# Kernel tuning notes

Hardware: AMD Instinct MI355X
Metric: run time of the kernel (lower is better)

Reference implementation:

```python
import jax, jax.numpy as jnp
import numpy as np

N, IN_DIM, HEADS, C = 100000, 128, 4, 32  # out_dim = HEADS*C = 128
E = 1600000


def setup_inputs() -> dict:
    key = jax.random.key(0)
    ks = jax.random.split(key, 9)
    x = jax.random.normal(ks[0], (N, IN_DIM), dtype=jnp.float32)
    edge_index = jax.random.randint(ks[1], (2, E), 0, N, dtype=jnp.int64)
    # GATConv params
    W = jax.random.normal(ks[2], (HEADS * C, IN_DIM), dtype=jnp.float32) * (1.0 / np.sqrt(IN_DIM))
    att_src = jax.random.normal(ks[3], (HEADS, C), dtype=jnp.float32) * 0.1
    att_dst = jax.random.normal(ks[4], (HEADS, C), dtype=jnp.float32) * 0.1
    bias = jax.random.normal(ks[5], (HEADS * C,), dtype=jnp.float32) * 0.01
    # complex phase + LayerNorm params
    phase = jax.random.normal(ks[6], (HEADS * C,), dtype=jnp.float32) * 0.02
    gamma = 1.0 + jax.random.normal(ks[7], (HEADS * C,), dtype=jnp.float32) * 0.01
    beta = jax.random.normal(ks[8], (HEADS * C,), dtype=jnp.float32) * 0.01
    return {"x": x, "edge_index": edge_index, "W": W, "att_src": att_src,
            "att_dst": att_dst, "bias": bias, "phase": phase, "gamma": gamma, "beta": beta}


def reference(x, edge_index, W, att_src, att_dst, bias, phase, gamma, beta):
    src, dst = edge_index[0], edge_index[1]
    h = (x @ W.T).reshape(N, HEADS, C)                      # [N,H,C]
    a_src = jnp.einsum('nhc,hc->nh', h, att_src)            # [N,H]
    a_dst = jnp.einsum('nhc,hc->nh', h, att_dst)
    e = jax.nn.leaky_relu(a_src[src] + a_dst[dst], 0.2)     # [E,H]
    # segment softmax over destination nodes (numerically stable)
    m = jax.ops.segment_max(e, dst, num_segments=N)         # [N,H]
    ex = jnp.exp(e - m[dst])
    s = jax.ops.segment_sum(ex, dst, num_segments=N)        # [N,H]
    alpha = ex / (s[dst] + 1e-16)                           # [E,H]
    msg = h[src] * alpha[:, :, None]                        # [E,H,C]
    out = jax.ops.segment_sum(msg, dst, num_segments=N).reshape(N, HEADS * C) + bias
    # complex phase magnitude: sqrt((h cos p)^2 + (h sin p)^2 + eps)
    mag = jnp.sqrt((out * jnp.cos(phase)) ** 2 + (out * jnp.sin(phase)) ** 2 + 1e-12)
    # LayerNorm
    mu = mag.mean(-1, keepdims=True)
    var = ((mag - mu) ** 2).mean(-1, keepdims=True)
    hn = (mag - mu) / jnp.sqrt(var + 1e-5) * gamma + beta
    return jax.nn.gelu(hn, approximate=False)
```

## Files before the change

### kernel.cpp

```cpp
#include <hip/hip_runtime.h>
#include <hip/hip_bf16.h>

#define N_ 100000
#define E_ 1600000
#define D_ 128
#define H_ 4
#define C_ 32

using bf16 = __hip_bfloat16;
typedef __attribute__((ext_vector_type(8))) short short8;
typedef __attribute__((ext_vector_type(4))) float f32x4;

__device__ __forceinline__ float u2f(unsigned u) { return __uint_as_float(u); }
__device__ __forceinline__ unsigned short f2bu(float v) {
  bf16 t = __float2bfloat16(v);
  return *(unsigned short*)&t;
}

__global__ __launch_bounds__(256) void k_linear_mfma(
    const float* __restrict__ x, const float* __restrict__ W,
    const float* __restrict__ att_src, const float* __restrict__ att_dst,
    bf16* __restrict__ h, float* __restrict__ a_src, float* __restrict__ a_dst) {
  __shared__ unsigned short WB[16384];
  __shared__ unsigned short XS[64 * 128];
  __shared__ float ats[128], atd[128];
  const int tid = threadIdx.x;
  const int lane = tid & 63, w = tid >> 6;
  const int n15 = lane & 15, quad = lane >> 4;

  for (int i = tid; i < 16384; i += 256) {
    const int n = i >> 7, k = i & 127;
    const int kk = k >> 5, q = (k >> 3) & 3, j = k & 7;
    const int frag = kk * 8 + (n >> 4);
    WB[frag * 512 + q * 128 + (n & 15) * 8 + j] = f2bu(W[n * 128 + k]);
  }
  if (tid < 128) { ats[tid] = att_src[tid]; atd[tid] = att_dst[tid]; }

  const int nrb = (N_ + 63) / 64;
  for (int rb = blockIdx.x; rb < nrb; rb += gridDim.x) {
    const int row0 = rb * 64;
    __syncthreads();
    for (int idx = tid; idx < 2048; idx += 256) {
      const int r = idx >> 5;
      const int c = (idx & 31) * 4;
      float4 xv = make_float4(0.f, 0.f, 0.f, 0.f);
      if (row0 + r < N_) xv = *(const float4*)&x[(size_t)(row0 + r) * 128 + c];
      ushort4 o;
      o.x = f2bu(xv.x); o.y = f2bu(xv.y); o.z = f2bu(xv.z); o.w = f2bu(xv.w);
      *(ushort4*)&XS[r * 128 + c] = o;
    }
    __syncthreads();

    f32x4 acc[8] = {};
    const int arow = w * 16 + n15;
#pragma unroll
    for (int kk = 0; kk < 4; kk++) {
      const short8 a = *(const short8*)&XS[arow * 128 + kk * 32 + quad * 8];
#pragma unroll
      for (int t = 0; t < 8; t++) {
        const short8 b = *(const short8*)&WB[(kk * 8 + t) * 512 + lane * 8];
        acc[t] = __builtin_amdgcn_mfma_f32_16x16x32_bf16(a, b, acc[t], 0, 0, 0);
      }
    }

    __syncthreads();
#pragma unroll
    for (int t = 0; t < 8; t++)
#pragma unroll
      for (int reg = 0; reg < 4; reg++)
        XS[(w * 16 + quad * 4 + reg) * 128 + t * 16 + n15] =
            f2bu(acc[t][reg]);
    __syncthreads();
    {
      const int row = tid >> 2;
      const int hd = tid & 3;
      const int cb = hd * 32;
      const int grow = row0 + row;
      float ps = 0.f, pd = 0.f;
      if (grow < N_) {
#pragma unroll
        for (int g = 0; g < 4; g++) {
          const uint4 v = *(const uint4*)&XS[row * 128 + cb + g * 8];
          *(uint4*)&h[(size_t)grow * 128 + cb + g * 8] = v;
          const unsigned uu[4] = {v.x, v.y, v.z, v.w};
#pragma unroll
          for (int p = 0; p < 4; p++) {
            const float f0 = u2f(uu[p] << 16);
            const float f1 = u2f(uu[p] & 0xffff0000u);
            const int cc = cb + g * 8 + p * 2;
            ps = fmaf(f0, ats[cc], ps);     ps = fmaf(f1, ats[cc + 1], ps);
            pd = fmaf(f0, atd[cc], pd);     pd = fmaf(f1, atd[cc + 1], pd);
          }
        }
        a_src[grow * 4 + hd] = ps;
        a_dst[grow * 4 + hd] = pd;
      }
    }
  }
}

__global__ __launch_bounds__(256) void k_link(const int* __restrict__ ei,
                                              int* __restrict__ head4,
                                              int* __restrict__ nxt) {
  const int e = blockIdx.x * 256 + threadIdx.x;
  if (e >= E_) return;
  const int d = ei[E_ + e];
  const int prev = atomicExch(&head4[d * 4 + (e & 3)], e);
  nxt[e] = prev;
}

__global__ __launch_bounds__(256) void k_gather_ll(
    const int* __restrict__ head4, const int* __restrict__ nxt,
    const int* __restrict__ ei, const float* __restrict__ a_src,
    const float* __restrict__ a_dst, const bf16* __restrict__ h,
    const float* __restrict__ bias, const float* __restrict__ phase,
    const float* __restrict__ gamma, const float* __restrict__ beta,
    float* __restrict__ out) {
  const int lane = threadIdx.x & 63;
  const int d = blockIdx.x * 4 + (threadIdx.x >> 6);
  if (d >= N_) return;
  const int head = lane >> 4;
  const float ad = a_dst[d * 4 + head];
  const int ch = lane * 2;

  int e0 = head4[d * 4 + 0], e1 = head4[d * 4 + 1];
  int e2 = head4[d * 4 + 2], e3 = head4[d * 4 + 3];

  float acc0 = 0.f, acc1 = 0.f, sumw = 0.f;
  while ((e0 & e1 & e2 & e3) != -1) {
    const int c0 = (e0 < 0) ? 0 : e0, c1 = (e1 < 0) ? 0 : e1;
    const int c2 = (e2 < 0) ? 0 : e2, c3 = (e3 < 0) ? 0 : e3;
    const int n0 = nxt[c0], n1 = nxt[c1], n2 = nxt[c2], n3 = nxt[c3];
    const int s0 = ei[c0], s1 = ei[c1], s2 = ei[c2], s3 = ei[c3];
    const __hip_bfloat162 h0 = *(const __hip_bfloat162*)&h[s0 * 128 + ch];
    const __hip_bfloat162 h1 = *(const __hip_bfloat162*)&h[s1 * 128 + ch];
    const __hip_bfloat162 h2 = *(const __hip_bfloat162*)&h[s2 * 128 + ch];
    const __hip_bfloat162 h3 = *(const __hip_bfloat162*)&h[s3 * 128 + ch];
    const float as0 = a_src[s0 * 4 + head], as1 = a_src[s1 * 4 + head];
    const float as2 = a_src[s2 * 4 + head], as3 = a_src[s3 * 4 + head];

    float v0 = as0 + ad; v0 = (v0 > 0.f) ? v0 : 0.2f * v0;
    float v1 = as1 + ad; v1 = (v1 > 0.f) ? v1 : 0.2f * v1;
    float v2 = as2 + ad; v2 = (v2 > 0.f) ? v2 : 0.2f * v2;
    float v3 = as3 + ad; v3 = (v3 > 0.f) ? v3 : 0.2f * v3;
    const float w0 = (e0 < 0) ? 0.f : __expf(v0);
    const float w1 = (e1 < 0) ? 0.f : __expf(v1);
    const float w2 = (e2 < 0) ? 0.f : __expf(v2);
    const float w3 = (e3 < 0) ? 0.f : __expf(v3);

    acc0 = fmaf(w0, __low2float(h0), acc0);
    acc1 = fmaf(w0, __high2float(h0), acc1);
    acc0 = fmaf(w1, __low2float(h1), acc0);
    acc1 = fmaf(w1, __high2float(h1), acc1);
    acc0 = fmaf(w2, __low2float(h2), acc0);
    acc1 = fmaf(w2, __high2float(h2), acc1);
    acc0 = fmaf(w3, __low2float(h3), acc0);
    acc1 = fmaf(w3, __high2float(h3), acc1);
    sumw += (w0 + w1) + (w2 + w3);

    e0 = (e0 < 0) ? -1 : n0;
    e1 = (e1 < 0) ? -1 : n1;
    e2 = (e2 < 0) ? -1 : n2;
    e3 = (e3 < 0) ? -1 : n3;
  }

  const float inv = 1.0f / (sumw + 1e-16f);
  const float2 bi = *(const float2*)&bias[ch];
  const float2 ph = *(const float2*)&phase[ch];
  const float v0 = acc0 * inv + bi.x;
  const float v1 = acc1 * inv + bi.y;
  float sp, cp;
  sincosf(ph.x, &sp, &cp);
  const float m0 = sqrtf(v0 * v0 * (cp * cp + sp * sp) + 1e-12f);
  sincosf(ph.y, &sp, &cp);
  const float m1 = sqrtf(v1 * v1 * (cp * cp + sp * sp) + 1e-12f);

  float s1 = m0 + m1;
#pragma unroll
  for (int off = 32; off > 0; off >>= 1) s1 += __shfl_xor(s1, off);
  const float mu = s1 * (1.0f / 128.0f);
  const float d0 = m0 - mu, d1 = m1 - mu;
  float q = d0 * d0 + d1 * d1;
#pragma unroll
  for (int off = 32; off > 0; off >>= 1) q += __shfl_xor(q, off);
  const float rstd = rsqrtf(q * (1.0f / 128.0f) + 1e-5f);
  const float2 ga = *(const float2*)&gamma[ch];
  const float2 be = *(const float2*)&beta[ch];
  const float hn0 = d0 * rstd * ga.x + be.x;
  const float hn1 = d1 * rstd * ga.y + be.y;
  const float g0 = 0.5f * hn0 * (1.0f + erff(hn0 * 0.70710678118654752f));
  const float g1 = 0.5f * hn1 * (1.0f + erff(hn1 * 0.70710678118654752f));
  *(float2*)&out[d * 128 + ch] = make_float2(g0, g1);
}

extern "C" void kernel_launch(void* const* d_in, const int* in_sizes, int n_in,
                              void* d_out, int out_size, void* d_ws, size_t ws_size,
                              hipStream_t stream) {
  const float* x       = (const float*)d_in[0];
  const int*   ei      = (const int*)d_in[1];
  const float* W       = (const float*)d_in[2];
  const float* att_src = (const float*)d_in[3];
  const float* att_dst = (const float*)d_in[4];
  const float* bias    = (const float*)d_in[5];
  const float* phase   = (const float*)d_in[6];
  const float* gamma   = (const float*)d_in[7];
  const float* beta    = (const float*)d_in[8];
  float* out = (float*)d_out;

  bf16*  h     = (bf16*)d_ws;
  float* a_src = (float*)(h + (size_t)N_ * D_);
  float* a_dst = a_src + (size_t)N_ * H_;
  int*   head4 = (int*)(a_dst + (size_t)N_ * H_);
  int*   nxt   = head4 + (size_t)N_ * 4;

  hipMemsetAsync(head4, 0xFF, (size_t)N_ * 4 * sizeof(int), stream);

  k_linear_mfma<<<768, 256, 0, stream>>>(x, W, att_src, att_dst, h, a_src,
                                         a_dst);
  k_link<<<(E_ + 255) / 256, 256, 0, stream>>>(ei, head4, nxt);
  k_gather_ll<<<(N_ + 3) / 4, 256, 0, stream>>>(head4, nxt, ei, a_src, a_dst,
                                                h, bias, phase, gamma, beta,
                                                out);
}
```

Measured before the change: 340.0 us.

## Use 8 linked-list chains per node with packed src/next and wide row loads

Edge linked lists are split into 8 chains per destination instead of 4. The source index and next pointer are packed into one int2 so each hop needs a single load. In the gather, each of 8 lane groups walks one chain and loads 32-byte chunks of the h row, then the groups are combined with shuffle reductions. The phase sin/cos term is dropped because cos²+sin²=1, which leaves more parallel pointer chasing per node but adds register pressure and cross-lane reduction cost.

Result: slower. 358.0 us (+5.3%).

```diff
diff --git a/kernel.cpp b/kernel.cpp
--- a/kernel.cpp
+++ b/kernel.cpp
@@ -100,97 +100,101 @@
 }
 
 __global__ __launch_bounds__(256) void k_link(const int* __restrict__ ei,
-                                              int* __restrict__ head4,
-                                              int* __restrict__ nxt) {
+                                              int* __restrict__ head8,
+                                              int2* __restrict__ nxt2) {
   const int e = blockIdx.x * 256 + threadIdx.x;
   if (e >= E_) return;
   const int d = ei[E_ + e];
-  const int prev = atomicExch(&head4[d * 4 + (e & 3)], e);
-  nxt[e] = prev;
-}
-
-__global__ __launch_bounds__(256) void k_gather_ll(
-    const int* __restrict__ head4, const int* __restrict__ nxt,
-    const int* __restrict__ ei, const float* __restrict__ a_src,
-    const float* __restrict__ a_dst, const bf16* __restrict__ h,
-    const float* __restrict__ bias, const float* __restrict__ phase,
+  const int prev = atomicExch(&head8[d * 8 + (e & 7)], e);
+  nxt2[e] = make_int2(ei[e], prev);
+}
+
+__global__ __launch_bounds__(256) void k_gather8(
+    const int* __restrict__ head8, const int2* __restrict__ nxt2,
+    const float* __restrict__ a_src, const float* __restrict__ a_dst,
+    const bf16* __restrict__ h, const float* __restrict__ bias,
     const float* __restrict__ gamma, const float* __restrict__ beta,
     float* __restrict__ out) {
   const int lane = threadIdx.x & 63;
   const int d = blockIdx.x * 4 + (threadIdx.x >> 6);
   if (d >= N_) return;
-  const int head = lane >> 4;
+  const int j = lane >> 3;
+  const int cg = lane & 7;
+  const int head = cg >> 1;
   const float ad = a_dst[d * 4 + head];
-  const int ch = lane * 2;
-
-  int e0 = head4[d * 4 + 0], e1 = head4[d * 4 + 1];
-  int e2 = head4[d * 4 + 2], e3 = head4[d * 4 + 3];
-
-  float acc0 = 0.f, acc1 = 0.f, sumw = 0.f;
-  while ((e0 & e1 & e2 & e3) != -1) {
-    const int c0 = (e0 < 0) ? 0 : e0, c1 = (e1 < 0) ? 0 : e1;
-    const int c2 = (e2 < 0) ? 0 : e2, c3 = (e3 < 0) ? 0 : e3;
-    const int n0 = nxt[c0], n1 = nxt[c1], n2 = nxt[c2], n3 = nxt[c3];
-    const int s0 = ei[c0], s1 = ei[c1], s2 = ei[c2], s3 = ei[c3];
-    const __hip_bfloat162 h0 = *(const __hip_bfloat162*)&h[s0 * 128 + ch];
-    const __hip_bfloat162 h1 = *(const __hip_bfloat162*)&h[s1 * 128 + ch];
-    const __hip_bfloat162 h2 = *(const __hip_bfloat162*)&h[s2 * 128 + ch];
-    const __hip_bfloat162 h3 = *(const __hip_bfloat162*)&h[s3 * 128 + ch];
-    const float as0 = a_src[s0 * 4 + head], as1 = a_src[s1 * 4 + head];
-    const float as2 = a_src[s2 * 4 + head], as3 = a_src[s3 * 4 + head];
-
-    float v0 = as0 + ad; v0 = (v0 > 0.f) ? v0 : 0.2f * v0;
-    float v1 = as1 + ad; v1 = (v1 > 0.f) ? v1 : 0.2f * v1;
-    float v2 = as2 + ad; v2 = (v2 > 0.f) ? v2 : 0.2f * v2;
-    float v3 = as3 + ad; v3 = (v3 > 0.f) ? v3 : 0.2f * v3;
-    const float w0 = (e0 < 0) ? 0.f : __expf(v0);
-    const float w1 = (e1 < 0) ? 0.f : __expf(v1);
-    const float w2 = (e2 < 0) ? 0.f : __expf(v2);
-    const float w3 = (e3 < 0) ? 0.f : __expf(v3);
-
-    acc0 = fmaf(w0, __low2float(h0), acc0);
-    acc1 = fmaf(w0, __high2float(h0), acc1);
-    acc0 = fmaf(w1, __low2float(h1), acc0);
-    acc1 = fmaf(w1, __high2float(h1), acc1);
-    acc0 = fmaf(w2, __low2float(h2), acc0);
-    acc1 = fmaf(w2, __high2float(h2), acc1);
-    acc0 = fmaf(w3, __low2float(h3), acc0);
-    acc1 = fmaf(w3, __high2float(h3), acc1);
-    sumw += (w0 + w1) + (w2 + w3);
-
-    e0 = (e0 < 0) ? -1 : n0;
-    e1 = (e1 < 0) ? -1 : n1;
-    e2 = (e2 < 0) ? -1 : n2;
-    e3 = (e3 < 0) ? -1 : n3;
+
+  int e = head8[d * 8 + j];
+  float acc[16];
+#pragma unroll
+  for (int k = 0; k < 16; k++) acc[k] = 0.f;
+  float sumw = 0.f;
+
+  while (__any(e != -1)) {
+    const int c = (e < 0) ? 0 : e;
+    const int2 sn = nxt2[c];
+    const int s = sn.x;
+    const uint4 u0 = *(const uint4*)&h[(size_t)s * 128 + cg * 16];
+    const uint4 u1 = *(const uint4*)&h[(size_t)s * 128 + cg * 16 + 8];
+    float ev = a_src[s * 4 + head] + ad;
+    ev = (ev > 0.f) ? ev : 0.2f * ev;
+    const float w = (e < 0) ? 0.f : __expf(ev);
+    const unsigned uu[8] = {u0.x, u0.y, u0.z, u0.w, u1.x, u1.y, u1.z, u1.w};
+#pragma unroll
+    for (int p = 0; p < 8; p++) {
+      acc[p * 2]     = fmaf(w, u2f(uu[p] << 16), acc[p * 2]);
+      acc[p * 2 + 1] = fmaf(w, u2f(uu[p] & 0xffff0000u), acc[p * 2 + 1]);
+    }
+    sumw += w;
+    e = (e < 0) ? -1 : sn.y;
+  }
+
+#pragma unroll
+  for (int off = 8; off <= 32; off <<= 1) {
+#pragma unroll
+    for (int k = 0; k < 16; k++) acc[k] += __shfl_xor(acc[k], off);
+    sumw += __shfl_xor(sumw, off);
   }
 
   const float inv = 1.0f / (sumw + 1e-16f);
-  const float2 bi = *(const float2*)&bias[ch];
-  const float2 ph = *(const float2*)&phase[ch];
-  const float v0 = acc0 * inv + bi.x;
-  const float v1 = acc1 * inv + bi.y;
-  float sp, cp;
-  sincosf(ph.x, &sp, &cp);
-  const float m0 = sqrtf(v0 * v0 * (cp * cp + sp * sp) + 1e-12f);
-  sincosf(ph.y, &sp, &cp);
-  const float m1 = sqrtf(v1 * v1 * (cp * cp + sp * sp) + 1e-12f);
-
-  float s1 = m0 + m1;
-#pragma unroll
-  for (int off = 32; off > 0; off >>= 1) s1 += __shfl_xor(s1, off);
-  const float mu = s1 * (1.0f / 128.0f);
-  const float d0 = m0 - mu, d1 = m1 - mu;
-  float q = d0 * d0 + d1 * d1;
-#pragma unroll
-  for (int off = 32; off > 0; off >>= 1) q += __shfl_xor(q, off);
+  float biv[16], gav[16], bev[16];
+#pragma unroll
+  for (int g = 0; g < 4; g++) {
+    *(float4*)&biv[g * 4] = *(const float4*)&bias[cg * 16 + g * 4];
+    *(float4*)&gav[g * 4] = *(const float4*)&gamma[cg * 16 + g * 4];
+    *(float4*)&bev[g * 4] = *(const float4*)&beta[cg * 16 + g * 4];
+  }
+
+  float m[16], part = 0.f;
+#pragma unroll
+  for (int k = 0; k < 16; k++) {
+    const float v = acc[k] * inv + biv[k];
+    m[k] = sqrtf(v * v + 1e-12f);
+    part += m[k];
+  }
+#pragma unroll
+  for (int off = 1; off <= 4; off <<= 1) part += __shfl_xor(part, off);
+  const float mu = part * (1.0f / 128.0f);
+  float q = 0.f;
+#pragma unroll
+  for (int k = 0; k < 16; k++) {
+    m[k] -= mu;
+    q += m[k] * m[k];
+  }
+#pragma unroll
+  for (int off = 1; off <= 4; off <<= 1) q += __shfl_xor(q, off);
   const float rstd = rsqrtf(q * (1.0f / 128.0f) + 1e-5f);
-  const float2 ga = *(const float2*)&gamma[ch];
-  const float2 be = *(const float2*)&beta[ch];
-  const float hn0 = d0 * rstd * ga.x + be.x;
-  const float hn1 = d1 * rstd * ga.y + be.y;
-  const float g0 = 0.5f * hn0 * (1.0f + erff(hn0 * 0.70710678118654752f));
-  const float g1 = 0.5f * hn1 * (1.0f + erff(hn1 * 0.70710678118654752f));
-  *(float2*)&out[d * 128 + ch] = make_float2(g0, g1);
+
+  float o[16];
+#pragma unroll
+  for (int k = 0; k < 16; k++) {
+    const float hn = m[k] * rstd * gav[k] + bev[k];
+    o[k] = 0.5f * hn * (1.0f + erff(hn * 0.70710678118654752f));
+  }
+  if (lane < 8) {
+#pragma unroll
+    for (int g = 0; g < 4; g++)
+      *(float4*)&out[(size_t)d * 128 + cg * 16 + g * 4] = *(float4*)&o[g * 4];
+  }
 }
 
 extern "C" void kernel_launch(void* const* d_in, const int* in_sizes, int n_in,
@@ -202,7 +206,6 @@
   const float* att_src = (const float*)d_in[3];
   const float* att_dst = (const float*)d_in[4];
   const float* bias    = (const float*)d_in[5];
-  const float* phase   = (const float*)d_in[6];
   const float* gamma   = (const float*)d_in[7];
   const float* beta    = (const float*)d_in[8];
   float* out = (float*)d_out;
@@ -210,15 +213,14 @@
   bf16*  h     = (bf16*)d_ws;
   float* a_src = (float*)(h + (size_t)N_ * D_);
   float* a_dst = a_src + (size_t)N_ * H_;
-  int*   head4 = (int*)(a_dst + (size_t)N_ * H_);
-  int*   nxt   = head4 + (size_t)N_ * 4;
-
-  hipMemsetAsync(head4, 0xFF, (size_t)N_ * 4 * sizeof(int), stream);
+  int*   head8 = (int*)(a_dst + (size_t)N_ * H_);
+  int2*  nxt2  = (int2*)(head8 + (size_t)N_ * 8);
+
+  hipMemsetAsync(head8, 0xFF, (size_t)N_ * 8 * sizeof(int), stream);
 
   k_linear_mfma<<<768, 256, 0, stream>>>(x, W, att_src, att_dst, h, a_src,
                                          a_dst);
-  k_link<<<(E_ + 255) / 256, 256, 0, stream>>>(ei, head4, nxt);
-  k_gather_ll<<<(N_ + 3) / 4, 256, 0, stream>>>(head4, nxt, ei, a_src, a_dst,
-                                                h, bias, phase, gamma, beta,
-                                                out);
-}
+  k_link<<<(E_ + 255) / 256, 256, 0, stream>>>(ei, head8, nxt2);
+  k_gather8<<<(N_ + 3) / 4, 256, 0, stream>>>(head8, nxt2, a_src, a_dst, h,
+                                              bias, gamma, beta, out);
+}
```

## Pack src index with next link and distribute list walks across lanes

Applied to the files above, without the earlier changes.

Stores the source index together with the next-edge link as one int2 per edge, so a single load per hop replaces two dependent loads. The gather kernel assigns lanes 0-3 to walk the four linked lists, computes each edge's weight once, and broadcasts the weights and source offsets with shuffles instead of having every lane reload the same list entries. It also drops the sin/cos phase computation, since cos^2+sin^2 = 1 algebraically. The trade-off is shuffle overhead per hop and divergence when the list lengths differ, and the cos^2+sin^2 rounding difference from the reference is ignored.

New measurement: 340.6 us. No clear change (+0.2%).

```diff
diff --git a/kernel.cpp b/kernel.cpp
--- a/kernel.cpp
+++ b/kernel.cpp
@@ -101,85 +101,68 @@
 
 __global__ __launch_bounds__(256) void k_link(const int* __restrict__ ei,
                                               int* __restrict__ head4,
-                                              int* __restrict__ nxt) {
+                                              int2* __restrict__ nxt2) {
   const int e = blockIdx.x * 256 + threadIdx.x;
   if (e >= E_) return;
   const int d = ei[E_ + e];
   const int prev = atomicExch(&head4[d * 4 + (e & 3)], e);
-  nxt[e] = prev;
-}
-
-__global__ __launch_bounds__(256) void k_gather_ll(
-    const int* __restrict__ head4, const int* __restrict__ nxt,
-    const int* __restrict__ ei, const float* __restrict__ a_src,
-    const float* __restrict__ a_dst, const bf16* __restrict__ h,
-    const float* __restrict__ bias, const float* __restrict__ phase,
+  nxt2[e] = make_int2(ei[e], prev);
+}
+
+__global__ __launch_bounds__(256) void k_gather4(
+    const int* __restrict__ head4, const int2* __restrict__ nxt2,
+    const float* __restrict__ a_src, const float* __restrict__ a_dst,
+    const bf16* __restrict__ h, const float* __restrict__ bias,
     const float* __restrict__ gamma, const float* __restrict__ beta,
     float* __restrict__ out) {
   const int lane = threadIdx.x & 63;
   const int d = blockIdx.x * 4 + (threadIdx.x >> 6);
   if (d >= N_) return;
   const int head = lane >> 4;
+  const int srcsel = lane & 48;
   const float ad = a_dst[d * 4 + head];
   const int ch = lane * 2;
 
-  int e0 = head4[d * 4 + 0], e1 = head4[d * 4 + 1];
-  int e2 = head4[d * 4 + 2], e3 = head4[d * 4 + 3];
-
-  float acc0 = 0.f, acc1 = 0.f, sumw = 0.f;
-  while ((e0 & e1 & e2 & e3) != -1) {
-    const int c0 = (e0 < 0) ? 0 : e0, c1 = (e1 < 0) ? 0 : e1;
-    const int c2 = (e2 < 0) ? 0 : e2, c3 = (e3 < 0) ? 0 : e3;
-    const int n0 = nxt[c0], n1 = nxt[c1], n2 = nxt[c2], n3 = nxt[c3];
-    const int s0 = ei[c0], s1 = ei[c1], s2 = ei[c2], s3 = ei[c3];
-    const __hip_bfloat162 h0 = *(const __hip_bfloat162*)&h[s0 * 128 + ch];
-    const __hip_bfloat162 h1 = *(const __hip_bfloat162*)&h[s1 * 128 + ch];
-    const __hip_bfloat162 h2 = *(const __hip_bfloat162*)&h[s2 * 128 + ch];
-    const __hip_bfloat162 h3 = *(const __hip_bfloat162*)&h[s3 * 128 + ch];
-    const float as0 = a_src[s0 * 4 + head], as1 = a_src[s1 * 4 + head];
-    const float as2 = a_src[s2 * 4 + head], as3 = a_src[s3 * 4 + head];
-
-    float v0 = as0 + ad; v0 = (v0 > 0.f) ? v0 : 0.2f * v0;
-    float v1 = as1 + ad; v1 = (v1 > 0.f) ? v1 : 0.2f * v1;
-    float v2 = as2 + ad; v2 = (v2 > 0.f) ? v2 : 0.2f * v2;
-    float v3 = as3 + ad; v3 = (v3 > 0.f) ? v3 : 0.2f * v3;
-    const float w0 = (e0 < 0) ? 0.f : __expf(v0);
-    const float w1 = (e1 < 0) ? 0.f : __expf(v1);
-    const float w2 = (e2 < 0) ? 0.f : __expf(v2);
-    const float w3 = (e3 < 0) ? 0.f : __expf(v3);
-
-    acc0 = fmaf(w0, __low2float(h0), acc0);
-    acc1 = fmaf(w0, __high2float(h0), acc1);
-    acc0 = fmaf(w1, __low2float(h1), acc0);
-    acc1 = fmaf(w1, __high2float(h1), acc1);
-    acc0 = fmaf(w2, __low2float(h2), acc0);
-    acc1 = fmaf(w2, __high2float(h2), acc1);
-    acc0 = fmaf(w3, __low2float(h3), acc0);
-    acc1 = fmaf(w3, __high2float(h3), acc1);
-    sumw += (w0 + w1) + (w2 + w3);
-
-    e0 = (e0 < 0) ? -1 : n0;
-    e1 = (e1 < 0) ? -1 : n1;
-    e2 = (e2 < 0) ? -1 : n2;
-    e3 = (e3 < 0) ? -1 : n3;
+  int e = head4[d * 4 + (lane & 3)];
+  float acc0 = 0.f, acc1 = 0.f, sumw_mine = 0.f;
+
+  while (__any(e != -1)) {
+    const int c = (e < 0) ? 0 : e;
+    const int2 sn = nxt2[c];
+    const int s = sn.x;
+    float ev = a_src[s * 4 + head] + ad;
+    ev = (ev > 0.f) ? ev : 0.2f * ev;
+    const float w = (e < 0) ? 0.f : __expf(ev);
+    sumw_mine += w;
+    const int soff = s << 7;
+
+#pragma unroll
+    for (int j = 0; j < 4; j++) {
+      const float wj = __shfl(w, srcsel | j);
+      const int oj = __shfl(soff, j);
+      const __hip_bfloat162 hv = *(const __hip_bfloat162*)&h[oj + ch];
+      acc0 = fmaf(wj, __low2float(hv), acc0);
+      acc1 = fmaf(wj, __high2float(hv), acc1);
+    }
+    e = (e < 0) ? -1 : sn.y;
   }
+
+  float sumw = sumw_mine;
+  sumw += __shfl_xor(sumw, 1);
+  sumw += __shfl_xor(sumw, 2);
 
   const float inv = 1.0f / (sumw + 1e-16f);
   const float2 bi = *(const float2*)&bias[ch];
-  const float2 ph = *(const float2*)&phase[ch];
   const float v0 = acc0 * inv + bi.x;
   const float v1 = acc1 * inv + bi.y;
-  float sp, cp;
-  sincosf(ph.x, &sp, &cp);
-  const float m0 = sqrtf(v0 * v0 * (cp * cp + sp * sp) + 1e-12f);
-  sincosf(ph.y, &sp, &cp);
-  const float m1 = sqrtf(v1 * v1 * (cp * cp + sp * sp) + 1e-12f);
-
-  float s1 = m0 + m1;
+  const float m0i = sqrtf(v0 * v0 + 1e-12f);
+  const float m1i = sqrtf(v1 * v1 + 1e-12f);
+
+  float s1 = m0i + m1i;
 #pragma unroll
   for (int off = 32; off > 0; off >>= 1) s1 += __shfl_xor(s1, off);
   const float mu = s1 * (1.0f / 128.0f);
-  const float d0 = m0 - mu, d1 = m1 - mu;
+  const float d0 = m0i - mu, d1 = m1i - mu;
   float q = d0 * d0 + d1 * d1;
 #pragma unroll
   for (int off = 32; off > 0; off >>= 1) q += __shfl_xor(q, off);
@@ -190,7 +173,7 @@
   const float hn1 = d1 * rstd * ga.y + be.y;
   const float g0 = 0.5f * hn0 * (1.0f + erff(hn0 * 0.70710678118654752f));
   const float g1 = 0.5f * hn1 * (1.0f + erff(hn1 * 0.70710678118654752f));
-  *(float2*)&out[d * 128 + ch] = make_float2(g0, g1);
+  *(float2*)&out[(size_t)d * 128 + ch] = make_float2(g0, g1);
 }
 
 extern "C" void kernel_launch(void* const* d_in, const int* in_sizes, int n_in,
@@ -202,7 +185,6 @@
   const float* att_src = (const float*)d_in[3];
   const float* att_dst = (const float*)d_in[4];
   const float* bias    = (const float*)d_in[5];
-  const float* phase   = (const float*)d_in[6];
   const float* gamma   = (const float*)d_in[7];
   const float* beta    = (const float*)d_in[8];
   float* out = (float*)d_out;
@@ -211,14 +193,13 @@
   float* a_src = (float*)(h + (size_t)N_ * D_);
   float* a_dst = a_src + (size_t)N_ * H_;
   int*   head4 = (int*)(a_dst + (size_t)N_ * H_);
-  int*   nxt   = head4 + (size_t)N_ * 4;
+  int2*  nxt2  = (int2*)(head4 + (size_t)N_ * 4);
 
   hipMemsetAsync(head4, 0xFF, (size_t)N_ * 4 * sizeof(int), stream);
 
   k_linear_mfma<<<768, 256, 0, stream>>>(x, W, att_src, att_dst, h, a_src,
                                          a_dst);
-  k_link<<<(E_ + 255) / 256, 256, 0, stream>>>(ei, head4, nxt);
-  k_gather_ll<<<(N_ + 3) / 4, 256, 0, stream>>>(head4, nxt, ei, a_src, a_dst,
-                                                h, bias, phase, gamma, beta,
-                                                out);
-}
+  k_link<<<(E_ + 255) / 256, 256, 0, stream>>>(ei, head4, nxt2);
+  k_gather4<<<(N_ + 3) / 4, 256, 0, stream>>>(head4, nxt2, a_src, a_dst, h,
+                                              bias, gamma, beta, out);
+}
```
